# Kernel optimization log

Measured on AMD Instinct MI355X. Metric: run time of the kernel, lower is better.

Reference implementation:

```python
import jax, jax.numpy as jnp
import numpy as np

B, L, E, H, W = 2, 4096, 512, 8, 128
D = E // H

def _clin(x, Wr, Wi, br, bi):
    # ComplexLinear on real input: out = x@(Wr + i*Wi)^T + (br + i*bi)
    return x @ Wr.T + br, x @ Wi.T + bi

def setup_inputs() -> dict:
    key = jax.random.key(0)
    ks = jax.random.split(key, 20)
    s = 0.02
    d = {
        'query': jax.random.normal(ks[0], (B, L, E), jnp.float32),
        'key':   jax.random.normal(ks[1], (B, L, E), jnp.float32),
        'value': jax.random.normal(ks[2], (B, L, E), jnp.float32),
    }
    names = ['q', 'k', 'v', 'o']
    i = 3
    for n in names:
        d[n + 'Wr'] = jax.random.normal(ks[i], (E, E), jnp.float32) * s; i += 1
        d[n + 'Wi'] = jax.random.normal(ks[i], (E, E), jnp.float32) * s; i += 1
        d[n + 'br'] = jnp.zeros((E,), jnp.float32)
        d[n + 'bi'] = jnp.zeros((E,), jnp.float32)
    return d

def reference(query, key, value,
              qWr, qWi, qbr, qbi,
              kWr, kWi, kbr, kbi,
              vWr, vWi, vbr, vbi,
              oWr, oWi, obr, obi):
    # complex projections (real input -> complex output, kept as (re, im) float pairs)
    qr, qi = _clin(query, qWr, qWi, qbr, qbi)
    kr, ki = _clin(key,   kWr, kWi, kbr, kbi)
    vr, _vi = _clin(value, vWr, vWi, vbr, vbi)  # imag part of V is discarded by the real cast

    def heads(x):
        return x.reshape(B, L, H, D).transpose(0, 2, 1, 3)  # [B,H,L,D]
    qr, qi, kr, ki, vr = map(heads, (qr, qi, kr, ki, vr))

    # Re(q @ k^H) = qr@kr^T + qi@ki^T  (only the real part is ever used)
    scale = 1.0 / np.sqrt(D)
    scores = (jnp.einsum('bhld,bhmd->bhlm', qr, kr)
              + jnp.einsum('bhld,bhmd->bhlm', qi, ki)) * scale

    # Faithful to source: only lower_mask is applied (window_mask is built but never added).
    idx = jnp.arange(L)
    lower_mask = jnp.where(idx[:, None] - idx[None, :] >= W + 1,
                           -jnp.inf, 0.0).astype(scores.dtype)
    probs = jax.nn.softmax(scores + lower_mask, axis=-1)

    # out = probs @ v; cast to query.dtype keeps only Re = probs @ vr
    o = jnp.einsum('bhlm,bhmd->bhld', probs, vr)
    o = o.transpose(0, 2, 1, 3).reshape(B, L, E)

    out_r = o @ oWr.T + obr
    out_i = o @ oWi.T + obi
    return out_r, out_i
```

## Files before the change

### kernel.cpp

```cpp
#include <hip/hip_runtime.h>


typedef unsigned short u16;
typedef unsigned int u32;
typedef __attribute__((ext_vector_type(8))) short bf16x8;
typedef __attribute__((ext_vector_type(4))) float f32x4;
typedef __attribute__((ext_vector_type(16))) float f32x16;
typedef __attribute__((ext_vector_type(4))) u32 u32x4;

#define L_ 4096
#define E_ 512
#define M_ 8192

__device__ __forceinline__ u16 f2bf(float f) {
  union { float f; u32 u; } v; v.f = f;
  return (u16)((v.u + 0x7FFFu + ((v.u >> 16) & 1u)) >> 16);
}

__device__ __forceinline__ void gll16(const void* g, void* l) {
  __builtin_amdgcn_global_load_lds(
      (const __attribute__((address_space(1))) u32*)g,
      (__attribute__((address_space(3))) u32*)l, 16, 0, 0);
}

__global__ void cvt_x_kernel(const float* __restrict__ q, const float* __restrict__ k,
                             const float* __restrict__ v,
                             u16* __restrict__ xq, u16* __restrict__ xk, u16* __restrict__ xv) {
  const int total = 3 * (M_ * E_ / 4);
  int stride = gridDim.x * blockDim.x;
  for (int u = blockIdx.x * blockDim.x + threadIdx.x; u < total; u += stride) {
    int mat = u >> 20, e = u & ((1 << 20) - 1);
    const float4 f = ((const float4*)(mat == 0 ? q : mat == 1 ? k : v))[e];
    ushort4 o = make_ushort4(f2bf(f.x), f2bf(f.y), f2bf(f.z), f2bf(f.w));
    *(ushort4*)((mat == 0 ? xq : mat == 1 ? xk : xv) + (size_t)e * 4) = o;
  }
}

struct CPtrs { const float* w[7]; const float* b[7]; };

__global__ void cvt_wb_kernel(CPtrs p, u16* __restrict__ wcat, float* __restrict__ bcat) {
  const int total = 7 * (E_ * E_ / 4);
  int stride = gridDim.x * blockDim.x;
  int t0 = blockIdx.x * blockDim.x + threadIdx.x;
  for (int u = t0; u < total; u += stride) {
    int wi = u >> 16, e = u & 65535;
    const float4 f = ((const float4*)p.w[wi])[e];
    ushort4 o = make_ushort4(f2bf(f.x), f2bf(f.y), f2bf(f.z), f2bf(f.w));
    *(ushort4*)(wcat + (size_t)wi * 262144 + (size_t)e * 4) = o;
  }
  for (int j = t0; j < 3584; j += stride) bcat[j] = p.b[j >> 9][j & 511];
}

__device__ __forceinline__ void gemm128_main(const u16* __restrict__ A, const u16* __restrict__ Bw,
                                             int m0, int n0w, char* sm, f32x4 acc[4][4]) {
  int tid = threadIdx.x;
  int lane = tid & 63, w = tid >> 6;
  int wm = w >> 1, wn = w & 1;
#pragma unroll
  for (int a = 0; a < 4; a++)
#pragma unroll
    for (int b = 0; b < 4; b++)
#pragma unroll
      for (int j = 0; j < 4; j++) acc[a][b][j] = 0.f;

  auto stage = [&](int buf, int ks) {
    char* dst = sm + buf * 16384;
#pragma unroll
    for (int n = 0; n < 2; n++) {
      int u = n * 256 + tid;
      int row = u >> 2, c = u & 3;
      int so = (c ^ (row & 3)) * 16;
      int ldso = (n * 256 + w * 64) * 16;
      gll16((const char*)(A + (size_t)(m0 + row) * 512 + ks * 32) + so, dst + ldso);
      gll16((const char*)(Bw + (size_t)(n0w + row) * 512 + ks * 32) + so, dst + 8192 + ldso);
    }
  };

  stage(0, 0);
  __syncthreads();
  int cur = 0;
  for (int ks = 0; ks < 16; ks++) {
    if (ks < 15) stage(cur ^ 1, ks + 1);
    const char* as = sm + cur * 16384;
    const char* bs = as + 8192;
    bf16x8 af[4], bfr[4];
#pragma unroll
    for (int i = 0; i < 4; i++) {
      int ra = wm * 64 + i * 16 + (lane & 15);
      af[i] = *(const bf16x8*)(as + ra * 64 + (((lane >> 4) * 16) ^ ((ra & 3) << 4)));
      int rb = wn * 64 + i * 16 + (lane & 15);
      bfr[i] = *(const bf16x8*)(bs + rb * 64 + (((lane >> 4) * 16) ^ ((rb & 3) << 4)));
    }
    __builtin_amdgcn_s_setprio(1);
#pragma unroll
    for (int mt = 0; mt < 4; mt++)
#pragma unroll
      for (int nt = 0; nt < 4; nt++)
        acc[mt][nt] = __builtin_amdgcn_mfma_f32_16x16x32_bf16(af[mt], bfr[nt], acc[mt][nt], 0, 0, 0);
    __builtin_amdgcn_s_setprio(0);
    __syncthreads();
    cur ^= 1;
  }
}

__global__ __launch_bounds__(256) void proj_kernel(
    const u16* __restrict__ xq, const u16* __restrict__ xk, const u16* __restrict__ xv,
    const u16* __restrict__ wcat, const float* __restrict__ bcat,
    u16* __restrict__ qrb, u16* __restrict__ qib,
    u16* __restrict__ krb, u16* __restrict__ kib, u16* __restrict__ vtb) {
  __shared__ alignas(16) char sm[32768];
  int bx = blockIdx.x, by = blockIdx.y;
  const u16* A = bx < 8 ? xq : (bx < 16 ? xk : xv);
  int m0 = by * 128, n0w = bx * 128;
  f32x4 acc[4][4];
  gemm128_main(A, wcat, m0, n0w, sm, acc);

  int lane = threadIdx.x & 63, w = threadIdx.x >> 6;
  int wm = w >> 1, wn = w & 1;
  int lL = lane & 15, lH = lane >> 4;
#pragma unroll
  for (int mt = 0; mt < 4; mt++) {
#pragma unroll
    for (int nt = 0; nt < 4; nt++) {
      int n = n0w + wn * 64 + nt * 16 + lL;
      float bias = bcat[n];
      int e = n & 511;
#pragma unroll
      for (int j = 0; j < 4; j++) {
        int m = m0 + wm * 64 + mt * 16 + lH * 4 + j;
        float val = acc[mt][nt][j] + bias;
        int bb = m >> 12, ll = m & 4095;
        if (bx < 16) {
          if (bx < 8) val *= 0.18033688011112042f;
          u16* dst = (bx < 8) ? ((n & 512) ? qib : qrb) : ((n & 512) ? kib : krb);
          dst[((size_t)((bb * 8 + (e >> 6)) * 4096 + ll) << 6) + (e & 63)] = f2bf(val);
        } else {
          vtb[((size_t)((bb * 8 + (e >> 6)) * 64 + (e & 63)) << 12) + ll] = f2bf(val);
        }
      }
    }
  }
}

__global__ __launch_bounds__(256) void oproj_kernel(
    const u16* __restrict__ obf, const u16* __restrict__ wcat, const float* __restrict__ bcat,
    float* __restrict__ out) {
  __shared__ alignas(16) char sm[32768];
  int bx = blockIdx.x, by = blockIdx.y;
  int m0 = by * 128, n0w = 2560 + bx * 128;
  f32x4 acc[4][4];
  gemm128_main(obf, wcat, m0, n0w, sm, acc);

  int lane = threadIdx.x & 63, w = threadIdx.x >> 6;
  int wm = w >> 1, wn = w & 1;
  int lL = lane & 15, lH = lane >> 4;
#pragma unroll
  for (int mt = 0; mt < 4; mt++) {
#pragma unroll
    for (int nt = 0; nt < 4; nt++) {
      int n = n0w + wn * 64 + nt * 16 + lL;
      float bias = bcat[n];
      int nn = n - 2560;
      float* dst = out + ((nn & 512) ? 4194304 : 0) + (nn & 511);
#pragma unroll
      for (int j = 0; j < 4; j++) {
        int m = m0 + wm * 64 + mt * 16 + lH * 4 + j;
        dst[(size_t)m * 512] = acc[mt][nt][j] + bias;
      }
    }
  }
}

__global__ __launch_bounds__(512, 4) void attn_kernel(
    const u16* __restrict__ qrb, const u16* __restrict__ qib,
    const u16* __restrict__ krb, const u16* __restrict__ kib,
    const u16* __restrict__ vtb, u16* __restrict__ obf) {
  __shared__ alignas(16) char sm[73728];
  int bid = blockIdx.x;
  int bh = bid & 15;
  int q2 = bid >> 4;
  int qt = (q2 < 16) ? q2 : (47 - q2);
  int bb = bh >> 3, hh = bh & 7;
  int i0 = qt << 7;
  int tid = threadIdx.x;
  int lane = tid & 63, w = tid >> 6;
  int grp = w >> 2, wq = w & 3;
  int lo = lane & 31, hi = lane >> 5;
  int i0w = i0 + wq * 32;
  int irow = i0w + lo;

  int jstart = (i0 >= 128) ? (i0 - 128) : 0;
  int ntiles = (4096 - jstart) >> 5;
  int nper = ntiles >> 1;

  bf16x8 fqr[4], fqi[4];
  {
    const u16* qp = qrb + ((size_t)(bh * 4096 + irow) << 6) + hi * 8;
    const u16* qip = qib + ((size_t)(bh * 4096 + irow) << 6) + hi * 8;
#pragma unroll
    for (int c = 0; c < 4; c++) {
      fqr[c] = *(const bf16x8*)(qp + c * 16);
      fqi[c] = *(const bf16x8*)(qip + c * 16);
    }
  }

  const char* gp[3];
  int adv[3], ldso[3];
  {
    const char* krbB = (const char*)krb + ((size_t)(bh * 4096 + jstart) << 7);
    const char* kibB = (const char*)kib + ((size_t)(bh * 4096 + jstart) << 7);
    const char* vtbB = (const char*)vtb + ((size_t)(bh * 64) << 13) + ((size_t)jstart << 1);
    int tI = grp;
#pragma unroll
    for (int s = 0; s < 3; s++) {
      int cc = 3 * w + s;
      int c12 = cc - 12 * tI;
      ldso[s] = cc * 1024;
      if (c12 < 8) {
        int r = (c12 & 3) * 8 + (lane >> 3);
        int so = ((lane & 7) ^ (r & 7)) << 4;
        gp[s] = (c12 < 4 ? krbB : kibB) + (size_t)(tI * 32 + r) * 128 + so;
        adv[s] = 8192;
      } else {
        int dr = (c12 - 8) * 16 + (lane >> 2);
        int so = ((lane & 3) ^ (dr & 3)) << 4;
        gp[s] = vtbB + (size_t)dr * 8192 + tI * 64 + so;
        adv[s] = 128;
      }
    }
  }
  auto stagep = [&](char* sb) {
#pragma unroll
    for (int s = 0; s < 3; s++) {
      gll16(gp[s], sb + ldso[s]);
      gp[s] += adv[s];
    }
  };

  int offK[4], offV[2];
#pragma unroll
  for (int c = 0; c < 4; c++) offK[c] = lo * 128 + ((c * 32 + hi * 16) ^ ((lo & 7) << 4));
#pragma unroll
  for (int kc = 0; kc < 2; kc++) offV[kc] = 8192 + lo * 64 + ((kc * 32 + hi * 16) ^ ((lo & 3) << 4));

  auto cvtpk = [](float a, float b) -> u32 {
    u32 r;
    asm("v_cvt_pk_bf16_f32 %0, %1, %2" : "=v"(r) : "v"(a), "v"(b));
    return r;
  };

  f32x16 oa0, oa1;
#pragma unroll
  for (int r = 0; r < 16; r++) { oa0[r] = 0.f; oa1[r] = 0.f; }
  float l_run = 0.f;
  const int iband = irow - 129;

  stagep(sm);
  __syncthreads();
  char* rb = sm + grp * 12288;
  char* sb = sm + 24576;
  int j0 = jstart + grp * 32;

  for (int p = 0; p < nper; p++) {
    if (p + 1 < nper) {
      stagep(sb);
      sb += 24576; if (sb == sm + 73728) sb = sm;
    }
    f32x16 s0;
#pragma unroll
    for (int r = 0; r < 16; r++) s0[r] = 0.f;
#pragma unroll
    for (int c = 0; c < 4; c++) {
      bf16x8 ar = *(const bf16x8*)(rb + offK[c]);
      bf16x8 ai = *(const bf16x8*)(rb + 4096 + offK[c]);
      __builtin_amdgcn_s_setprio(1);
      s0 = __builtin_amdgcn_mfma_f32_32x32x16_bf16(ar, fqr[c], s0, 0, 0, 0);
      s0 = __builtin_amdgcn_mfma_f32_32x32x16_bf16(ai, fqi[c], s0, 0, 0, 0);
      __builtin_amdgcn_s_setprio(0);
    }
    if (j0 <= i0w - 98) {
#pragma unroll
      for (int r = 0; r < 16; r++) {
        int kk = j0 + (r & 3) + ((r >> 2) << 3) + (hi << 2);
        if (kk <= iband) s0[r] = -3e38f;
      }
    }
    float ps0 = 0.f, ps1 = 0.f, ps2 = 0.f, ps3 = 0.f;
#pragma unroll
    for (int r = 0; r < 16; r += 4) {
      s0[r] = exp2f(s0[r]);         ps0 += s0[r];
      s0[r + 1] = exp2f(s0[r + 1]); ps1 += s0[r + 1];
      s0[r + 2] = exp2f(s0[r + 2]); ps2 += s0[r + 2];
      s0[r + 3] = exp2f(s0[r + 3]); ps3 += s0[r + 3];
    }
    float psum = (ps0 + ps1) + (ps2 + ps3);
    psum += __shfl_xor(psum, 32);
    l_run += psum;

    bf16x8 pf0, pf1;
    {
      const float* pp = (const float*)&s0;
      u32 x0 = cvtpk(pp[0], pp[1]), y0 = cvtpk(pp[4], pp[5]);
      u32 x1 = cvtpk(pp[2], pp[3]), y1 = cvtpk(pp[6], pp[7]);
      u32 x2 = cvtpk(pp[8], pp[9]), y2 = cvtpk(pp[12], pp[13]);
      u32 x3 = cvtpk(pp[10], pp[11]), y3 = cvtpk(pp[14], pp[15]);
      asm("v_permlane32_swap_b32 %0, %1" : "+v"(x0), "+v"(y0));
      asm("v_permlane32_swap_b32 %0, %1" : "+v"(x1), "+v"(y1));
      asm("v_permlane32_swap_b32 %0, %1" : "+v"(x2), "+v"(y2));
      asm("v_permlane32_swap_b32 %0, %1" : "+v"(x3), "+v"(y3));
      u32x4 a; a[0] = x0; a[1] = x1; a[2] = y0; a[3] = y1;
      u32x4 b; b[0] = x2; b[1] = x3; b[2] = y2; b[3] = y3;
      pf0 = __builtin_bit_cast(bf16x8, a);
      pf1 = __builtin_bit_cast(bf16x8, b);
    }
    {
      bf16x8 av00 = *(const bf16x8*)(rb + offV[0]);
      bf16x8 av01 = *(const bf16x8*)(rb + offV[0] + 2048);
      bf16x8 av10 = *(const bf16x8*)(rb + offV[1]);
      bf16x8 av11 = *(const bf16x8*)(rb + offV[1] + 2048);
      __builtin_amdgcn_s_setprio(1);
      oa0 = __builtin_amdgcn_mfma_f32_32x32x16_bf16(av00, pf0, oa0, 0, 0, 0);
      oa1 = __builtin_amdgcn_mfma_f32_32x32x16_bf16(av01, pf0, oa1, 0, 0, 0);
      oa0 = __builtin_amdgcn_mfma_f32_32x32x16_bf16(av10, pf1, oa0, 0, 0, 0);
      oa1 = __builtin_amdgcn_mfma_f32_32x32x16_bf16(av11, pf1, oa1, 0, 0, 0);
      __builtin_amdgcn_s_setprio(0);
    }
    rb += 24576; if (rb >= sm + 73728) rb -= 73728;
    j0 += 64;
    __syncthreads();
  }

  int swo = (lo & 7) << 4;
  char* ob = sm + wq * 8192;
  if (grp == 1) {
#pragma unroll
    for (int g2 = 0; g2 < 4; g2++) {
      f32x4 v0; f32x4 v1;
#pragma unroll
      for (int e = 0; e < 4; e++) { v0[e] = oa0[4 * g2 + e]; v1[e] = oa1[4 * g2 + e]; }
      *(f32x4*)(ob + lo * 256 + ((g2 * 32 + hi * 16) ^ swo)) = v0;
      *(f32x4*)(ob + lo * 256 + ((128 + g2 * 32 + hi * 16) ^ swo)) = v1;
    }
    if (!hi) *(float*)(sm + 32768 + wq * 128 + lo * 4) = l_run;
  }
  __syncthreads();
  if (grp == 0) {
    float l2 = *(const float*)(sm + 32768 + wq * 128 + lo * 4);
    float rl = 1.0f / (l_run + l2);
    u16* orow = obf + ((size_t)(bb * 4096 + irow) << 9) + hh * 64;
#pragma unroll
    for (int g2 = 0; g2 < 4; g2++) {
      f32x4 v0 = *(const f32x4*)(ob + lo * 256 + ((g2 * 32 + hi * 16) ^ swo));
      f32x4 v1 = *(const f32x4*)(ob + lo * 256 + ((128 + g2 * 32 + hi * 16) ^ swo));
      ushort4 o0 = make_ushort4(f2bf((oa0[4 * g2] + v0[0]) * rl),
                                f2bf((oa0[4 * g2 + 1] + v0[1]) * rl),
                                f2bf((oa0[4 * g2 + 2] + v0[2]) * rl),
                                f2bf((oa0[4 * g2 + 3] + v0[3]) * rl));
      *(ushort4*)(orow + g2 * 8 + hi * 4) = o0;
      ushort4 o1 = make_ushort4(f2bf((oa1[4 * g2] + v1[0]) * rl),
                                f2bf((oa1[4 * g2 + 1] + v1[1]) * rl),
                                f2bf((oa1[4 * g2 + 2] + v1[2]) * rl),
                                f2bf((oa1[4 * g2 + 3] + v1[3]) * rl));
      *(ushort4*)(orow + 32 + g2 * 8 + hi * 4) = o1;
    }
  }
}

extern "C" void kernel_launch(void* const* d_in, const int* in_sizes, int n_in,
                              void* d_out, int out_size, void* d_ws, size_t ws_size,
                              hipStream_t stream) {
  (void)in_sizes; (void)n_in; (void)out_size; (void)ws_size;
  const float* q = (const float*)d_in[0];
  const float* k = (const float*)d_in[1];
  const float* v = (const float*)d_in[2];
  char* ws = (char*)d_ws;
  u16* wcat = (u16*)(ws + 0x000000);
  float* bcat = (float*)(ws + 0x400000);
  u16* xq  = (u16*)(ws + 0x500000);
  u16* xk  = (u16*)(ws + 0xD00000);
  u16* xv  = (u16*)(ws + 0x1500000);
  u16* qrb = (u16*)(ws + 0x1D00000);
  u16* qib = (u16*)(ws + 0x2500000);
  u16* krb = (u16*)(ws + 0x2D00000);
  u16* kib = (u16*)(ws + 0x3500000);
  u16* vtb = (u16*)(ws + 0x3D00000);
  u16* obf = xq;
  float* out = (float*)d_out;

  cvt_x_kernel<<<2048, 256, 0, stream>>>(q, k, v, xq, xk, xv);

  CPtrs cp;
  cp.w[0] = (const float*)d_in[3];  cp.w[1] = (const float*)d_in[4];
  cp.w[2] = (const float*)d_in[7];  cp.w[3] = (const float*)d_in[8];
  cp.w[4] = (const float*)d_in[11]; cp.w[5] = (const float*)d_in[15]; cp.w[6] = (const float*)d_in[16];
  cp.b[0] = (const float*)d_in[5];  cp.b[1] = (const float*)d_in[6];
  cp.b[2] = (const float*)d_in[9];  cp.b[3] = (const float*)d_in[10];
  cp.b[4] = (const float*)d_in[13]; cp.b[5] = (const float*)d_in[17]; cp.b[6] = (const float*)d_in[18];
  cvt_wb_kernel<<<448, 256, 0, stream>>>(cp, wcat, bcat);

  proj_kernel<<<dim3(20, 64), 256, 0, stream>>>(xq, xk, xv, wcat, bcat, qrb, qib, krb, kib, vtb);
  attn_kernel<<<512, 512, 0, stream>>>(qrb, qib, krb, kib, vtb, obf);
  oproj_kernel<<<dim3(8, 64), 256, 0, stream>>>(obf, wcat, bcat, out);
}
```

Baseline: 174.8 us.

## Split attention key range across two segments per block and merge partials

Each attention block now handles two query tiles (jj and 31-jj), processing half of each tile's key range, and writes unnormalized fp32 partial outputs and row sums to scratch (the output buffer and workspace). A new merge kernel sums the two halves, normalizes, and writes bf16 for the output projection. The intent is to balance work per block, since causal-band tile lengths vary widely, at the cost of extra fp32 partial traffic and an additional kernel launch.

```diff
diff --git a/kernel.cpp b/kernel.cpp
--- a/kernel.cpp
+++ b/kernel.cpp
@@ -174,68 +174,15 @@
 __global__ __launch_bounds__(512, 4) void attn_kernel(
     const u16* __restrict__ qrb, const u16* __restrict__ qib,
     const u16* __restrict__ krb, const u16* __restrict__ kib,
-    const u16* __restrict__ vtb, u16* __restrict__ obf) {
+    const u16* __restrict__ vtb, float* __restrict__ pO, float* __restrict__ pl) {
   __shared__ alignas(16) char sm[73728];
   int bid = blockIdx.x;
   int bh = bid & 15;
-  int q2 = bid >> 4;
-  int qt = (q2 < 16) ? q2 : (47 - q2);
-  int bb = bh >> 3, hh = bh & 7;
-  int i0 = qt << 7;
+  int jj = bid >> 4;
   int tid = threadIdx.x;
   int lane = tid & 63, w = tid >> 6;
   int grp = w >> 2, wq = w & 3;
   int lo = lane & 31, hi = lane >> 5;
-  int i0w = i0 + wq * 32;
-  int irow = i0w + lo;
-
-  int jstart = (i0 >= 128) ? (i0 - 128) : 0;
-  int ntiles = (4096 - jstart) >> 5;
-  int nper = ntiles >> 1;
-
-  bf16x8 fqr[4], fqi[4];
-  {
-    const u16* qp = qrb + ((size_t)(bh * 4096 + irow) << 6) + hi * 8;
-    const u16* qip = qib + ((size_t)(bh * 4096 + irow) << 6) + hi * 8;
-#pragma unroll
-    for (int c = 0; c < 4; c++) {
-      fqr[c] = *(const bf16x8*)(qp + c * 16);
-      fqi[c] = *(const bf16x8*)(qip + c * 16);
-    }
-  }
-
-  const char* gp[3];
-  int adv[3], ldso[3];
-  {
-    const char* krbB = (const char*)krb + ((size_t)(bh * 4096 + jstart) << 7);
-    const char* kibB = (const char*)kib + ((size_t)(bh * 4096 + jstart) << 7);
-    const char* vtbB = (const char*)vtb + ((size_t)(bh * 64) << 13) + ((size_t)jstart << 1);
-    int tI = grp;
-#pragma unroll
-    for (int s = 0; s < 3; s++) {
-      int cc = 3 * w + s;
-      int c12 = cc - 12 * tI;
-      ldso[s] = cc * 1024;
-      if (c12 < 8) {
-        int r = (c12 & 3) * 8 + (lane >> 3);
-        int so = ((lane & 7) ^ (r & 7)) << 4;
-        gp[s] = (c12 < 4 ? krbB : kibB) + (size_t)(tI * 32 + r) * 128 + so;
-        adv[s] = 8192;
-      } else {
-        int dr = (c12 - 8) * 16 + (lane >> 2);
-        int so = ((lane & 3) ^ (dr & 3)) << 4;
-        gp[s] = vtbB + (size_t)dr * 8192 + tI * 64 + so;
-        adv[s] = 128;
-      }
-    }
-  }
-  auto stagep = [&](char* sb) {
-#pragma unroll
-    for (int s = 0; s < 3; s++) {
-      gll16(gp[s], sb + ldso[s]);
-      gp[s] += adv[s];
-    }
-  };
 
   int offK[4], offV[2];
 #pragma unroll
@@ -249,121 +196,193 @@
     return r;
   };
 
-  f32x16 oa0, oa1;
-#pragma unroll
-  for (int r = 0; r < 16; r++) { oa0[r] = 0.f; oa1[r] = 0.f; }
-  float l_run = 0.f;
-  const int iband = irow - 129;
-
-  stagep(sm);
-  __syncthreads();
-  char* rb = sm + grp * 12288;
-  char* sb = sm + 24576;
-  int j0 = jstart + grp * 32;
-
-  for (int p = 0; p < nper; p++) {
-    if (p + 1 < nper) {
-      stagep(sb);
-      sb += 24576; if (sb == sm + 73728) sb = sm;
-    }
-    f32x16 s0;
-#pragma unroll
-    for (int r = 0; r < 16; r++) s0[r] = 0.f;
-#pragma unroll
-    for (int c = 0; c < 4; c++) {
-      bf16x8 ar = *(const bf16x8*)(rb + offK[c]);
-      bf16x8 ai = *(const bf16x8*)(rb + 4096 + offK[c]);
-      __builtin_amdgcn_s_setprio(1);
-      s0 = __builtin_amdgcn_mfma_f32_32x32x16_bf16(ar, fqr[c], s0, 0, 0, 0);
-      s0 = __builtin_amdgcn_mfma_f32_32x32x16_bf16(ai, fqi[c], s0, 0, 0, 0);
-      __builtin_amdgcn_s_setprio(0);
-    }
-    if (j0 <= i0w - 98) {
-#pragma unroll
-      for (int r = 0; r < 16; r++) {
-        int kk = j0 + (r & 3) + ((r >> 2) << 3) + (hi << 2);
-        if (kk <= iband) s0[r] = -3e38f;
-      }
-    }
-    float ps0 = 0.f, ps1 = 0.f, ps2 = 0.f, ps3 = 0.f;
-#pragma unroll
-    for (int r = 0; r < 16; r += 4) {
-      s0[r] = exp2f(s0[r]);         ps0 += s0[r];
-      s0[r + 1] = exp2f(s0[r + 1]); ps1 += s0[r + 1];
-      s0[r + 2] = exp2f(s0[r + 2]); ps2 += s0[r + 2];
-      s0[r + 3] = exp2f(s0[r + 3]); ps3 += s0[r + 3];
-    }
-    float psum = (ps0 + ps1) + (ps2 + ps3);
-    psum += __shfl_xor(psum, 32);
-    l_run += psum;
-
-    bf16x8 pf0, pf1;
+  for (int seg = 0; seg < 2; seg++) {
+    int qt = seg ? (31 - jj) : jj;
+    int i0 = qt << 7;
+    int i0w = i0 + wq * 32;
+    int irow = i0w + lo;
+    int jsb = (i0 >= 128) ? (i0 - 128) : 0;
+    int T = (4096 - jsb) >> 5;
+    int half = T >> 1;
+    int jstart = jsb + (seg ? (half << 5) : 0);
+    int nper = half >> 1;
+
+    bf16x8 fqr[4], fqi[4];
     {
-      const float* pp = (const float*)&s0;
-      u32 x0 = cvtpk(pp[0], pp[1]), y0 = cvtpk(pp[4], pp[5]);
-      u32 x1 = cvtpk(pp[2], pp[3]), y1 = cvtpk(pp[6], pp[7]);
-      u32 x2 = cvtpk(pp[8], pp[9]), y2 = cvtpk(pp[12], pp[13]);
-      u32 x3 = cvtpk(pp[10], pp[11]), y3 = cvtpk(pp[14], pp[15]);
-      asm("v_permlane32_swap_b32 %0, %1" : "+v"(x0), "+v"(y0));
-      asm("v_permlane32_swap_b32 %0, %1" : "+v"(x1), "+v"(y1));
-      asm("v_permlane32_swap_b32 %0, %1" : "+v"(x2), "+v"(y2));
-      asm("v_permlane32_swap_b32 %0, %1" : "+v"(x3), "+v"(y3));
-      u32x4 a; a[0] = x0; a[1] = x1; a[2] = y0; a[3] = y1;
-      u32x4 b; b[0] = x2; b[1] = x3; b[2] = y2; b[3] = y3;
-      pf0 = __builtin_bit_cast(bf16x8, a);
-      pf1 = __builtin_bit_cast(bf16x8, b);
-    }
+      const u16* qp = qrb + ((size_t)(bh * 4096 + irow) << 6) + hi * 8;
+      const u16* qip = qib + ((size_t)(bh * 4096 + irow) << 6) + hi * 8;
+#pragma unroll
+      for (int c = 0; c < 4; c++) {
+        fqr[c] = *(const bf16x8*)(qp + c * 16);
+        fqi[c] = *(const bf16x8*)(qip + c * 16);
+      }
+    }
+
+    const char* gp[3];
+    int adv[3], ldso[3];
     {
-      bf16x8 av00 = *(const bf16x8*)(rb + offV[0]);
-      bf16x8 av01 = *(const bf16x8*)(rb + offV[0] + 2048);
-      bf16x8 av10 = *(const bf16x8*)(rb + offV[1]);
-      bf16x8 av11 = *(const bf16x8*)(rb + offV[1] + 2048);
-      __builtin_amdgcn_s_setprio(1);
-      oa0 = __builtin_amdgcn_mfma_f32_32x32x16_bf16(av00, pf0, oa0, 0, 0, 0);
-      oa1 = __builtin_amdgcn_mfma_f32_32x32x16_bf16(av01, pf0, oa1, 0, 0, 0);
-      oa0 = __builtin_amdgcn_mfma_f32_32x32x16_bf16(av10, pf1, oa0, 0, 0, 0);
-      oa1 = __builtin_amdgcn_mfma_f32_32x32x16_bf16(av11, pf1, oa1, 0, 0, 0);
-      __builtin_amdgcn_s_setprio(0);
-    }
-    rb += 24576; if (rb >= sm + 73728) rb -= 73728;
-    j0 += 64;
+      const char* krbB = (const char*)krb + ((size_t)(bh * 4096 + jstart) << 7);
+      const char* kibB = (const char*)kib + ((size_t)(bh * 4096 + jstart) << 7);
+      const char* vtbB = (const char*)vtb + ((size_t)(bh * 64) << 13) + ((size_t)jstart << 1);
+      int tI = grp;
+#pragma unroll
+      for (int s = 0; s < 3; s++) {
+        int cc = 3 * w + s;
+        int c12 = cc - 12 * tI;
+        ldso[s] = cc * 1024;
+        if (c12 < 8) {
+          int r = (c12 & 3) * 8 + (lane >> 3);
+          int so = ((lane & 7) ^ (r & 7)) << 4;
+          gp[s] = (c12 < 4 ? krbB : kibB) + (size_t)(tI * 32 + r) * 128 + so;
+          adv[s] = 8192;
+        } else {
+          int dr = (c12 - 8) * 16 + (lane >> 2);
+          int so = ((lane & 3) ^ (dr & 3)) << 4;
+          gp[s] = vtbB + (size_t)dr * 8192 + tI * 64 + so;
+          adv[s] = 128;
+        }
+      }
+    }
+    auto stagep = [&](char* sb) {
+#pragma unroll
+      for (int s = 0; s < 3; s++) {
+        gll16(gp[s], sb + ldso[s]);
+        gp[s] += adv[s];
+      }
+    };
+
+    f32x16 oa0, oa1;
+#pragma unroll
+    for (int r = 0; r < 16; r++) { oa0[r] = 0.f; oa1[r] = 0.f; }
+    float l_run = 0.f;
+    const int iband = irow - 129;
+
+    stagep(sm);
     __syncthreads();
-  }
-
-  int swo = (lo & 7) << 4;
-  char* ob = sm + wq * 8192;
-  if (grp == 1) {
-#pragma unroll
-    for (int g2 = 0; g2 < 4; g2++) {
-      f32x4 v0; f32x4 v1;
-#pragma unroll
-      for (int e = 0; e < 4; e++) { v0[e] = oa0[4 * g2 + e]; v1[e] = oa1[4 * g2 + e]; }
-      *(f32x4*)(ob + lo * 256 + ((g2 * 32 + hi * 16) ^ swo)) = v0;
-      *(f32x4*)(ob + lo * 256 + ((128 + g2 * 32 + hi * 16) ^ swo)) = v1;
-    }
-    if (!hi) *(float*)(sm + 32768 + wq * 128 + lo * 4) = l_run;
-  }
-  __syncthreads();
-  if (grp == 0) {
-    float l2 = *(const float*)(sm + 32768 + wq * 128 + lo * 4);
-    float rl = 1.0f / (l_run + l2);
-    u16* orow = obf + ((size_t)(bb * 4096 + irow) << 9) + hh * 64;
-#pragma unroll
-    for (int g2 = 0; g2 < 4; g2++) {
-      f32x4 v0 = *(const f32x4*)(ob + lo * 256 + ((g2 * 32 + hi * 16) ^ swo));
-      f32x4 v1 = *(const f32x4*)(ob + lo * 256 + ((128 + g2 * 32 + hi * 16) ^ swo));
-      ushort4 o0 = make_ushort4(f2bf((oa0[4 * g2] + v0[0]) * rl),
-                                f2bf((oa0[4 * g2 + 1] + v0[1]) * rl),
-                                f2bf((oa0[4 * g2 + 2] + v0[2]) * rl),
-                                f2bf((oa0[4 * g2 + 3] + v0[3]) * rl));
-      *(ushort4*)(orow + g2 * 8 + hi * 4) = o0;
-      ushort4 o1 = make_ushort4(f2bf((oa1[4 * g2] + v1[0]) * rl),
-                                f2bf((oa1[4 * g2 + 1] + v1[1]) * rl),
-                                f2bf((oa1[4 * g2 + 2] + v1[2]) * rl),
-                                f2bf((oa1[4 * g2 + 3] + v1[3]) * rl));
-      *(ushort4*)(orow + 32 + g2 * 8 + hi * 4) = o1;
-    }
-  }
+    char* rb = sm + grp * 12288;
+    char* sb = sm + 24576;
+    int j0 = jstart + grp * 32;
+
+    for (int p = 0; p < nper; p++) {
+      if (p + 1 < nper) {
+        stagep(sb);
+        sb += 24576; if (sb == sm + 73728) sb = sm;
+      }
+      f32x16 s0;
+#pragma unroll
+      for (int r = 0; r < 16; r++) s0[r] = 0.f;
+#pragma unroll
+      for (int c = 0; c < 4; c++) {
+        bf16x8 ar = *(const bf16x8*)(rb + offK[c]);
+        bf16x8 ai = *(const bf16x8*)(rb + 4096 + offK[c]);
+        __builtin_amdgcn_s_setprio(1);
+        s0 = __builtin_amdgcn_mfma_f32_32x32x16_bf16(ar, fqr[c], s0, 0, 0, 0);
+        s0 = __builtin_amdgcn_mfma_f32_32x32x16_bf16(ai, fqi[c], s0, 0, 0, 0);
+        __builtin_amdgcn_s_setprio(0);
+      }
+      if (j0 <= i0w - 98) {
+#pragma unroll
+        for (int r = 0; r < 16; r++) {
+          int kk = j0 + (r & 3) + ((r >> 2) << 3) + (hi << 2);
+          if (kk <= iband) s0[r] = -3e38f;
+        }
+      }
+      float ps0 = 0.f, ps1 = 0.f, ps2 = 0.f, ps3 = 0.f;
+#pragma unroll
+      for (int r = 0; r < 16; r += 4) {
+        s0[r] = exp2f(s0[r]);         ps0 += s0[r];
+        s0[r + 1] = exp2f(s0[r + 1]); ps1 += s0[r + 1];
+        s0[r + 2] = exp2f(s0[r + 2]); ps2 += s0[r + 2];
+        s0[r + 3] = exp2f(s0[r + 3]); ps3 += s0[r + 3];
+      }
+      float psum = (ps0 + ps1) + (ps2 + ps3);
+      psum += __shfl_xor(psum, 32);
+      l_run += psum;
+
+      bf16x8 pf0, pf1;
+      {
+        const float* pp = (const float*)&s0;
+        u32 x0 = cvtpk(pp[0], pp[1]), y0 = cvtpk(pp[4], pp[5]);
+        u32 x1 = cvtpk(pp[2], pp[3]), y1 = cvtpk(pp[6], pp[7]);
+        u32 x2 = cvtpk(pp[8], pp[9]), y2 = cvtpk(pp[12], pp[13]);
+        u32 x3 = cvtpk(pp[10], pp[11]), y3 = cvtpk(pp[14], pp[15]);
+        asm("v_permlane32_swap_b32 %0, %1" : "+v"(x0), "+v"(y0));
+        asm("v_permlane32_swap_b32 %0, %1" : "+v"(x1), "+v"(y1));
+        asm("v_permlane32_swap_b32 %0, %1" : "+v"(x2), "+v"(y2));
+        asm("v_permlane32_swap_b32 %0, %1" : "+v"(x3), "+v"(y3));
+        u32x4 a; a[0] = x0; a[1] = x1; a[2] = y0; a[3] = y1;
+        u32x4 b; b[0] = x2; b[1] = x3; b[2] = y2; b[3] = y3;
+        pf0 = __builtin_bit_cast(bf16x8, a);
+        pf1 = __builtin_bit_cast(bf16x8, b);
+      }
+      {
+        bf16x8 av00 = *(const bf16x8*)(rb + offV[0]);
+        bf16x8 av01 = *(const bf16x8*)(rb + offV[0] + 2048);
+        bf16x8 av10 = *(const bf16x8*)(rb + offV[1]);
+        bf16x8 av11 = *(const bf16x8*)(rb + offV[1] + 2048);
+        __builtin_amdgcn_s_setprio(1);
+        oa0 = __builtin_amdgcn_mfma_f32_32x32x16_bf16(av00, pf0, oa0, 0, 0, 0);
+        oa1 = __builtin_amdgcn_mfma_f32_32x32x16_bf16(av01, pf0, oa1, 0, 0, 0);
+        oa0 = __builtin_amdgcn_mfma_f32_32x32x16_bf16(av10, pf1, oa0, 0, 0, 0);
+        oa1 = __builtin_amdgcn_mfma_f32_32x32x16_bf16(av11, pf1, oa1, 0, 0, 0);
+        __builtin_amdgcn_s_setprio(0);
+      }
+      rb += 24576; if (rb >= sm + 73728) rb -= 73728;
+      j0 += 64;
+      __syncthreads();
+    }
+
+    int swo = (lo & 7) << 4;
+    char* ob = sm + wq * 8192;
+    if (grp == 1) {
+#pragma unroll
+      for (int g2 = 0; g2 < 4; g2++) {
+        f32x4 v0; f32x4 v1;
+#pragma unroll
+        for (int e = 0; e < 4; e++) { v0[e] = oa0[4 * g2 + e]; v1[e] = oa1[4 * g2 + e]; }
+        *(f32x4*)(ob + lo * 256 + ((g2 * 32 + hi * 16) ^ swo)) = v0;
+        *(f32x4*)(ob + lo * 256 + ((128 + g2 * 32 + hi * 16) ^ swo)) = v1;
+      }
+      if (!hi) *(float*)(sm + 32768 + wq * 128 + lo * 4) = l_run;
+    }
+    __syncthreads();
+    if (grp == 0) {
+      float l2 = *(const float*)(sm + 32768 + wq * 128 + lo * 4);
+      int prix = ((seg << 4) + bh) * 4096 + irow;
+      float* prow = pO + ((size_t)prix << 6);
+#pragma unroll
+      for (int g2 = 0; g2 < 4; g2++) {
+        f32x4 v0 = *(const f32x4*)(ob + lo * 256 + ((g2 * 32 + hi * 16) ^ swo));
+        f32x4 v1 = *(const f32x4*)(ob + lo * 256 + ((128 + g2 * 32 + hi * 16) ^ swo));
+        f32x4 o0, o1;
+#pragma unroll
+        for (int e = 0; e < 4; e++) {
+          o0[e] = oa0[4 * g2 + e] + v0[e];
+          o1[e] = oa1[4 * g2 + e] + v1[e];
+        }
+        *(f32x4*)(prow + g2 * 8 + hi * 4) = o0;
+        *(f32x4*)(prow + 32 + g2 * 8 + hi * 4) = o1;
+      }
+      if (!hi) pl[prix] = l_run + l2;
+    }
+    __syncthreads();
+  }
+}
+
+__global__ __launch_bounds__(256) void merge_kernel(const float* __restrict__ pO,
+                                                    const float* __restrict__ pl,
+                                                    u16* __restrict__ obf) {
+  int t = blockIdx.x * 256 + threadIdx.x;
+  int r = t >> 4;
+  int c = (t & 15) << 2;
+  float rl = 1.0f / (pl[r] + pl[65536 + r]);
+  f32x4 a = *(const f32x4*)(pO + ((size_t)r << 6) + c);
+  f32x4 b = *(const f32x4*)(pO + ((size_t)(65536 + r) << 6) + c);
+  int bh = r >> 12, q = r & 4095;
+  u16* dst = obf + ((size_t)((bh >> 3) * 4096 + q) << 9) + (bh & 7) * 64 + c;
+  ushort4 o = make_ushort4(f2bf((a[0] + b[0]) * rl), f2bf((a[1] + b[1]) * rl),
+                           f2bf((a[2] + b[2]) * rl), f2bf((a[3] + b[3]) * rl));
+  *(ushort4*)dst = o;
 }
 
 extern "C" void kernel_launch(void* const* d_in, const int* in_sizes, int n_in,
@@ -384,8 +403,10 @@
   u16* krb = (u16*)(ws + 0x2D00000);
   u16* kib = (u16*)(ws + 0x3500000);
   u16* vtb = (u16*)(ws + 0x3D00000);
+  float* pl = (float*)(ws + 0x4500000);
   u16* obf = xq;
   float* out = (float*)d_out;
+  float* pO = out;
 
   cvt_x_kernel<<<2048, 256, 0, stream>>>(q, k, v, xq, xk, xv);
 
@@ -399,6 +420,7 @@
   cvt_wb_kernel<<<448, 256, 0, stream>>>(cp, wcat, bcat);
 
   proj_kernel<<<dim3(20, 64), 256, 0, stream>>>(xq, xk, xv, wcat, bcat, qrb, qib, krb, kib, vtb);
-  attn_kernel<<<512, 512, 0, stream>>>(qrb, qib, krb, kib, vtb, obf);
+  attn_kernel<<<512, 512, 0, stream>>>(qrb, qib, krb, kib, vtb, pO, pl);
+  merge_kernel<<<4096, 256, 0, stream>>>(pO, pl, obf);
   oproj_kernel<<<dim3(8, 64), 256, 0, stream>>>(obf, wcat, bcat, out);
 }
```

New measurement: 195.5 us. 1.12x slower.

## Shrink attention block to 64 query rows with double-buffered shared K/V tiles

Applied to the files above, without the earlier changes.

Each attention block now covers 64 query rows with 4 waves instead of 128 rows with 8, which doubles the grid to 1024 blocks and drops the mirrored query-tile ordering. The shared-memory ring changes from three 24 KB stages to two alternating halves, and the V tile layout changes so both key groups read V from one shared tile. This is meant to improve load balance and occupancy, since the per-block iteration count varies with the causal-band start. The cost is twice the K/V traffic per query row and only two-stage prefetch depth.

```diff
diff --git a/kernel.cpp b/kernel.cpp
--- a/kernel.cpp
+++ b/kernel.cpp
@@ -171,20 +171,19 @@
   }
 }
 
-__global__ __launch_bounds__(512, 4) void attn_kernel(
+__global__ __launch_bounds__(256, 3) void attn_kernel(
     const u16* __restrict__ qrb, const u16* __restrict__ qib,
     const u16* __restrict__ krb, const u16* __restrict__ kib,
     const u16* __restrict__ vtb, u16* __restrict__ obf) {
-  __shared__ alignas(16) char sm[73728];
+  __shared__ alignas(16) char sm[49152];
   int bid = blockIdx.x;
   int bh = bid & 15;
-  int q2 = bid >> 4;
-  int qt = (q2 < 16) ? q2 : (47 - q2);
+  int qt = bid >> 4;
   int bb = bh >> 3, hh = bh & 7;
-  int i0 = qt << 7;
+  int i0 = qt << 6;
   int tid = threadIdx.x;
   int lane = tid & 63, w = tid >> 6;
-  int grp = w >> 2, wq = w & 3;
+  int grp = w >> 1, wq = w & 1;
   int lo = lane & 31, hi = lane >> 5;
   int i0w = i0 + wq * 32;
   int irow = i0w + lo;
@@ -204,44 +203,46 @@
     }
   }
 
-  const char* gp[3];
-  int adv[3], ldso[3];
+  const char* gp[6];
+  int adv[6], ldso[6];
   {
     const char* krbB = (const char*)krb + ((size_t)(bh * 4096 + jstart) << 7);
     const char* kibB = (const char*)kib + ((size_t)(bh * 4096 + jstart) << 7);
     const char* vtbB = (const char*)vtb + ((size_t)(bh * 64) << 13) + ((size_t)jstart << 1);
-    int tI = grp;
-#pragma unroll
-    for (int s = 0; s < 3; s++) {
-      int cc = 3 * w + s;
-      int c12 = cc - 12 * tI;
-      ldso[s] = cc * 1024;
-      if (c12 < 8) {
-        int r = (c12 & 3) * 8 + (lane >> 3);
+#pragma unroll
+    for (int s = 0; s < 6; s++) {
+      int cc = 6 * w + s;
+      ldso[s] = cc << 10;
+      if (cc < 16) {
+        int tI = cc >> 3;
+        int kind = (cc >> 2) & 1;
+        int r = (cc & 3) * 8 + (lane >> 3);
         int so = ((lane & 7) ^ (r & 7)) << 4;
-        gp[s] = (c12 < 4 ? krbB : kibB) + (size_t)(tI * 32 + r) * 128 + so;
+        gp[s] = (kind ? kibB : krbB) + (size_t)(tI * 32 + r) * 128 + so;
         adv[s] = 8192;
       } else {
-        int dr = (c12 - 8) * 16 + (lane >> 2);
-        int so = ((lane & 3) ^ (dr & 3)) << 4;
-        gp[s] = vtbB + (size_t)dr * 8192 + tI * 64 + so;
+        int dr = (cc - 16) * 8 + (lane >> 3);
+        int so = ((lane & 7) ^ (dr & 7)) << 4;
+        gp[s] = vtbB + (size_t)dr * 8192 + so;
         adv[s] = 128;
       }
     }
   }
-  auto stagep = [&](char* sb) {
-#pragma unroll
-    for (int s = 0; s < 3; s++) {
-      gll16(gp[s], sb + ldso[s]);
+  auto stagep = [&](char* dst) {
+#pragma unroll
+    for (int s = 0; s < 6; s++) {
+      gll16(gp[s], dst + ldso[s]);
       gp[s] += adv[s];
     }
   };
 
-  int offK[4], offV[2];
-#pragma unroll
-  for (int c = 0; c < 4; c++) offK[c] = lo * 128 + ((c * 32 + hi * 16) ^ ((lo & 7) << 4));
-#pragma unroll
-  for (int kc = 0; kc < 2; kc++) offV[kc] = 8192 + lo * 64 + ((kc * 32 + hi * 16) ^ ((lo & 3) << 4));
+  int swz = (lo & 7) << 4;
+  int offK[4], offVT[2];
+#pragma unroll
+  for (int c = 0; c < 4; c++) offK[c] = lo * 128 + ((c * 32 + hi * 16) ^ swz);
+#pragma unroll
+  for (int kc = 0; kc < 2; kc++)
+    offVT[kc] = 16384 + lo * 128 + ((grp * 64 + kc * 32 + hi * 16) ^ swz);
 
   auto cvtpk = [](float a, float b) -> u32 {
     u32 r;
@@ -257,31 +258,30 @@
 
   stagep(sm);
   __syncthreads();
-  char* rb = sm + grp * 12288;
-  char* sb = sm + 24576;
-  int j0 = jstart + grp * 32;
+  int j0g = jstart + grp * 32;
 
   for (int p = 0; p < nper; p++) {
-    if (p + 1 < nper) {
-      stagep(sb);
-      sb += 24576; if (sb == sm + 73728) sb = sm;
-    }
+    char* half = sm + (p & 1) * 24576;
+    if (p + 1 < nper) stagep(sm + ((p + 1) & 1) * 24576);
+    const char* Kr = half + grp * 8192;
+    const char* Ki = Kr + 4096;
+
     f32x16 s0;
 #pragma unroll
     for (int r = 0; r < 16; r++) s0[r] = 0.f;
 #pragma unroll
     for (int c = 0; c < 4; c++) {
-      bf16x8 ar = *(const bf16x8*)(rb + offK[c]);
-      bf16x8 ai = *(const bf16x8*)(rb + 4096 + offK[c]);
+      bf16x8 ar = *(const bf16x8*)(Kr + offK[c]);
+      bf16x8 ai = *(const bf16x8*)(Ki + offK[c]);
       __builtin_amdgcn_s_setprio(1);
       s0 = __builtin_amdgcn_mfma_f32_32x32x16_bf16(ar, fqr[c], s0, 0, 0, 0);
       s0 = __builtin_amdgcn_mfma_f32_32x32x16_bf16(ai, fqi[c], s0, 0, 0, 0);
       __builtin_amdgcn_s_setprio(0);
     }
-    if (j0 <= i0w - 98) {
+    if (j0g <= i0w - 98) {
 #pragma unroll
       for (int r = 0; r < 16; r++) {
-        int kk = j0 + (r & 3) + ((r >> 2) << 3) + (hi << 2);
+        int kk = j0g + (r & 3) + ((r >> 2) << 3) + (hi << 2);
         if (kk <= iband) s0[r] = -3e38f;
       }
     }
@@ -314,10 +314,10 @@
       pf1 = __builtin_bit_cast(bf16x8, b);
     }
     {
-      bf16x8 av00 = *(const bf16x8*)(rb + offV[0]);
-      bf16x8 av01 = *(const bf16x8*)(rb + offV[0] + 2048);
-      bf16x8 av10 = *(const bf16x8*)(rb + offV[1]);
-      bf16x8 av11 = *(const bf16x8*)(rb + offV[1] + 2048);
+      bf16x8 av00 = *(const bf16x8*)(half + offVT[0]);
+      bf16x8 av01 = *(const bf16x8*)(half + offVT[0] + 4096);
+      bf16x8 av10 = *(const bf16x8*)(half + offVT[1]);
+      bf16x8 av11 = *(const bf16x8*)(half + offVT[1] + 4096);
       __builtin_amdgcn_s_setprio(1);
       oa0 = __builtin_amdgcn_mfma_f32_32x32x16_bf16(av00, pf0, oa0, 0, 0, 0);
       oa1 = __builtin_amdgcn_mfma_f32_32x32x16_bf16(av01, pf0, oa1, 0, 0, 0);
@@ -325,8 +325,7 @@
       oa1 = __builtin_amdgcn_mfma_f32_32x32x16_bf16(av11, pf1, oa1, 0, 0, 0);
       __builtin_amdgcn_s_setprio(0);
     }
-    rb += 24576; if (rb >= sm + 73728) rb -= 73728;
-    j0 += 64;
+    j0g += 64;
     __syncthreads();
   }
 
@@ -341,11 +340,11 @@
       *(f32x4*)(ob + lo * 256 + ((g2 * 32 + hi * 16) ^ swo)) = v0;
       *(f32x4*)(ob + lo * 256 + ((128 + g2 * 32 + hi * 16) ^ swo)) = v1;
     }
-    if (!hi) *(float*)(sm + 32768 + wq * 128 + lo * 4) = l_run;
+    if (!hi) *(float*)(sm + 16384 + wq * 128 + lo * 4) = l_run;
   }
   __syncthreads();
   if (grp == 0) {
-    float l2 = *(const float*)(sm + 32768 + wq * 128 + lo * 4);
+    float l2 = *(const float*)(sm + 16384 + wq * 128 + lo * 4);
     float rl = 1.0f / (l_run + l2);
     u16* orow = obf + ((size_t)(bb * 4096 + irow) << 9) + hh * 64;
 #pragma unroll
@@ -399,6 +398,6 @@
   cvt_wb_kernel<<<448, 256, 0, stream>>>(cp, wcat, bcat);
 
   proj_kernel<<<dim3(20, 64), 256, 0, stream>>>(xq, xk, xv, wcat, bcat, qrb, qib, krb, kib, vtb);
-  attn_kernel<<<512, 512, 0, stream>>>(qrb, qib, krb, kib, vtb, obf);
+  attn_kernel<<<1024, 256, 0, stream>>>(qrb, qib, krb, kib, vtb, obf);
   oproj_kernel<<<dim3(8, 64), 256, 0, stream>>>(obf, wcat, bcat, out);
 }
```

New measurement: 178.7 us. +2.3%, slower.
